# Kernel tuning notes

Hardware: AMD Instinct MI355X
Metric: run time of the kernel (lower is better)

## Reference

```python
import jax, jax.numpy as jnp
import numpy as np

N_NODES = 50000
N_EDGES = 800000
F_IN = 16
F_EDGE = 8
H = 8  # latent_dim = [8, 8]
NUM_GRAPHS = 512


def setup_inputs() -> dict:
    key = jax.random.key(0)
    ks = jax.random.split(key, 16)
    x = jax.random.normal(ks[0], (N_NODES, F_IN), dtype=jnp.float32)
    edge_index = jax.random.randint(ks[1], (2, N_EDGES), 0, N_NODES)
    edge_attr = jax.random.normal(ks[2], (N_EDGES, F_EDGE), dtype=jnp.float32)
    batch = jnp.sort(jax.random.randint(ks[3], (N_NODES,), 0, NUM_GRAPHS))
    s = 0.1
    # edge MLPs (single Linear each): edge_attr -> flattened [in, out] weight
    We1 = jax.random.normal(ks[4], (F_EDGE, F_IN * H), dtype=jnp.float32) * s
    be1 = jnp.zeros((F_IN * H,), dtype=jnp.float32)
    We2 = jax.random.normal(ks[5], (F_EDGE, H * H), dtype=jnp.float32) * s
    be2 = jnp.zeros((H * H,), dtype=jnp.float32)
    # NNConv root weights + biases
    root1 = jax.random.normal(ks[6], (F_IN, H), dtype=jnp.float32) * s
    b1 = jnp.zeros((H,), dtype=jnp.float32)
    root2 = jax.random.normal(ks[7], (H, H), dtype=jnp.float32) * s
    b2 = jnp.zeros((H,), dtype=jnp.float32)
    # final readout linear H -> 1
    Wlast = jax.random.normal(ks[8], (H, 1), dtype=jnp.float32) * s
    blast = jnp.zeros((1,), dtype=jnp.float32)
    return {"x": x, "edge_index": edge_index, "edge_attr": edge_attr, "batch": batch,
            "We1": We1, "be1": be1, "root1": root1, "b1": b1,
            "We2": We2, "be2": be2, "root2": root2, "b2": b2,
            "Wlast": Wlast, "blast": blast}


def _nnconv(x, src, dst, edge_attr, We, be, root, b, in_dim, out_dim):
    # per-edge weight matrix from edge MLP: [E, in_dim, out_dim]
    W = (edge_attr @ We + be).reshape(-1, in_dim, out_dim)
    # gather source features, per-edge matvec, scatter-add to targets
    msg = jnp.einsum('ei,eio->eo', x[src], W)            # [E, out_dim]
    agg = jax.ops.segment_sum(msg, dst, num_segments=x.shape[0])
    return agg + x @ root + b                            # root weight + bias


def reference(x, edge_index, edge_attr, batch, We1, be1, root1, b1,
              We2, be2, root2, b2, Wlast, blast):
    src, dst = edge_index[0], edge_index[1]
    h = jax.nn.relu(_nnconv(x, src, dst, edge_attr, We1, be1, root1, b1, F_IN, H))
    h = jax.nn.relu(_nnconv(h, src, dst, edge_attr, We2, be2, root2, b2, H, H))
    # per-graph sum pooling (vectorized equivalent of the python loop)
    pooled = jax.ops.segment_sum(h, batch, num_segments=NUM_GRAPHS)  # [G, H]
    return pooled @ Wlast + blast                                    # [G, 1]
```

## Files before the change

kernel.cpp:

```cpp
#include <hip/hip_runtime.h>
#include <hip/hip_fp16.h>

#define F_EDGE 8
#define H 8

__device__ __forceinline__ unsigned short f2bf(float f) {
    unsigned u = __float_as_uint(f);
    unsigned r = u + 0x7fffu + ((u >> 16) & 1u);
    return (unsigned short)(r >> 16);
}
__device__ __forceinline__ float bflo(unsigned u) { return __uint_as_float(u << 16); }
__device__ __forceinline__ float bfhi(unsigned u) { return __uint_as_float(u & 0xffff0000u); }

__global__ void init_out_kernel(float* __restrict__ out,
                                const float* __restrict__ blast, int n) {
    int g = blockIdx.x * blockDim.x + threadIdx.x;
    if (g < n) out[g] = blast[0];
}

__global__ __launch_bounds__(256) void pack_edges_kernel(
    const int* __restrict__ ei, const float* __restrict__ ea,
    uint2* __restrict__ rec, int E) {
    int e = blockIdx.x * blockDim.x + threadIdx.x;
    if (e >= E) return;
    uint2 hdr;
    hdr.x = (unsigned)ei[e];
    hdr.y = (unsigned)ei[E + e];
    const float4* av = (const float4*)(ea + (size_t)e * F_EDGE);
    float4 a0 = av[0], a1 = av[1];
    uint2 p0, p1;
    p0.x = (unsigned)f2bf(a0.x) | ((unsigned)f2bf(a0.y) << 16);
    p0.y = (unsigned)f2bf(a0.z) | ((unsigned)f2bf(a0.w) << 16);
    p1.x = (unsigned)f2bf(a1.x) | ((unsigned)f2bf(a1.y) << 16);
    p1.y = (unsigned)f2bf(a1.z) | ((unsigned)f2bf(a1.w) << 16);
    size_t b = (size_t)e * 3;
    rec[b] = hdr;
    rec[b + 1] = p0;
    rec[b + 2] = p1;
}

template <int IN, bool RELU, bool F16IN>
__global__ __launch_bounds__(256) void prep_kernel(
    const void* __restrict__ featv, const float* __restrict__ We,
    const float* __restrict__ be, const float* __restrict__ root,
    const float* __restrict__ b, unsigned short* __restrict__ Pt,
    float* __restrict__ q, __half* __restrict__ seedh, int n_nodes) {
    __shared__ float sW[IN * H * 12];
    int tid = threadIdx.x;
    for (int t = tid; t < IN * H * 12; t += 256) {
        int r = t / 12, m = t - r * 12;
        float v = 0.f;
        if (m < 8) v = We[m * (IN * H) + r];
        else if (m == 8) v = be[r];
        else if (m == 9) v = root[r];
        sW[t] = v;
    }
    __syncthreads();

    int n = blockIdx.x * 32 + (tid >> 3);
    if (n >= n_nodes) return;
    int j = tid & 7;

    float f[IN];
    if (F16IN) {
        const uint4* fv = (const uint4*)((const unsigned short*)featv + (size_t)n * IN);
        uint4 v = fv[0];
        unsigned w[4] = {v.x, v.y, v.z, v.w};
#pragma unroll
        for (int p = 0; p < 4 && 2 * p + 1 < IN; ++p) {
            __half2 h2v = *(__half2*)&w[p];
            float2 ff = __half22float2(h2v);
            f[2 * p] = ff.x;
            f[2 * p + 1] = ff.y;
        }
    } else {
        const float4* fv = (const float4*)((const float*)featv + (size_t)n * IN);
#pragma unroll
        for (int i4 = 0; i4 < IN / 4; ++i4) {
            float4 v = fv[i4];
            f[i4 * 4 + 0] = v.x; f[i4 * 4 + 1] = v.y;
            f[i4 * 4 + 2] = v.z; f[i4 * 4 + 3] = v.w;
        }
    }
    if (RELU) {
#pragma unroll
        for (int i = 0; i < IN; ++i) f[i] = f[i] > 0.f ? f[i] : 0.f;
    }

    float p[8] = {0.f, 0.f, 0.f, 0.f, 0.f, 0.f, 0.f, 0.f};
    float qq = 0.f, hr = 0.f;
#pragma unroll
    for (int i = 0; i < IN; ++i) {
        const float* row = &sW[(i * 8 + j) * 12];
        float4 w0 = *(const float4*)row;
        float4 w1 = *(const float4*)(row + 4);
        float2 br = *(const float2*)(row + 8);
        float fi = f[i];
        p[0] = fmaf(fi, w0.x, p[0]); p[1] = fmaf(fi, w0.y, p[1]);
        p[2] = fmaf(fi, w0.z, p[2]); p[3] = fmaf(fi, w0.w, p[3]);
        p[4] = fmaf(fi, w1.x, p[4]); p[5] = fmaf(fi, w1.y, p[5]);
        p[6] = fmaf(fi, w1.z, p[6]); p[7] = fmaf(fi, w1.w, p[7]);
        qq = fmaf(fi, br.x, qq);
        hr = fmaf(fi, br.y, hr);
    }
    uint4 pw;
    pw.x = (unsigned)f2bf(p[0]) | ((unsigned)f2bf(p[1]) << 16);
    pw.y = (unsigned)f2bf(p[2]) | ((unsigned)f2bf(p[3]) << 16);
    pw.z = (unsigned)f2bf(p[4]) | ((unsigned)f2bf(p[5]) << 16);
    pw.w = (unsigned)f2bf(p[6]) | ((unsigned)f2bf(p[7]) << 16);
    *(uint4*)(Pt + ((long long)n * H + j) * F_EDGE) = pw;
    q[(long long)n * H + j] = qq;
    seedh[(long long)n * H + j] = __float2half(hr + b[j]);
}

__global__ __launch_bounds__(256) void edge_fact_kernel(
    const uint2* __restrict__ rec,
    const unsigned short* __restrict__ Pt,
    const float* __restrict__ q,
    __half* __restrict__ agg,
    int E) {
    long long gid = (long long)blockIdx.x * blockDim.x + threadIdx.x;
    int e = (int)(gid >> 2);
    if (e >= E) return;
    int jj = (int)(gid & 3);

    size_t rb = (size_t)e * 3;
    uint2 hdr = rec[rb];
    uint2 A = rec[rb + 1];
    uint2 B = rec[rb + 2];
    int src = (int)hdr.x;
    int dst = (int)hdr.y;

    float a0 = bflo(A.x), a1 = bfhi(A.x), a2 = bflo(A.y), a3 = bfhi(A.y);
    float a4 = bflo(B.x), a5 = bfhi(B.x), a6 = bflo(B.y), a7 = bfhi(B.y);

    const uint4* pp = (const uint4*)(Pt + (size_t)src * 64 + jj * 16);
    uint4 lo = pp[0];
    uint4 hi = pp[1];

    float2 q2 = *(const float2*)(q + (size_t)src * H + jj * 2);

    float m0 = q2.x;
    m0 = fmaf(a0, bflo(lo.x), m0); m0 = fmaf(a1, bfhi(lo.x), m0);
    m0 = fmaf(a2, bflo(lo.y), m0); m0 = fmaf(a3, bfhi(lo.y), m0);
    m0 = fmaf(a4, bflo(lo.z), m0); m0 = fmaf(a5, bfhi(lo.z), m0);
    m0 = fmaf(a6, bflo(lo.w), m0); m0 = fmaf(a7, bfhi(lo.w), m0);

    float m1 = q2.y;
    m1 = fmaf(a0, bflo(hi.x), m1); m1 = fmaf(a1, bfhi(hi.x), m1);
    m1 = fmaf(a2, bflo(hi.y), m1); m1 = fmaf(a3, bfhi(hi.y), m1);
    m1 = fmaf(a4, bflo(hi.z), m1); m1 = fmaf(a5, bfhi(hi.z), m1);
    m1 = fmaf(a6, bflo(hi.w), m1); m1 = fmaf(a7, bfhi(hi.w), m1);

    __half2* ap = (__half2*)agg + ((size_t)dst * 4 + jj);
    unsafeAtomicAdd(ap, __floats2half2_rn(m0, m1));
}

__global__ __launch_bounds__(256) void pool_kernel(
    const unsigned short* __restrict__ h2, const int* __restrict__ batch,
    const float* __restrict__ Wlast, float* __restrict__ out,
    int n_nodes, int n_graphs) {
    __shared__ float bins[512];
    bool use_bins = (n_graphs <= 512);
    if (use_bins) {
        for (int t = threadIdx.x; t < n_graphs; t += 256) bins[t] = 0.f;
        __syncthreads();
    }
    float wl[8];
#pragma unroll
    for (int j = 0; j < 8; ++j) wl[j] = Wlast[j];

    int base = blockIdx.x * 1024;
#pragma unroll
    for (int r = 0; r < 4; ++r) {
        int n = base + r * 256 + threadIdx.x;
        if (n < n_nodes) {
            uint4 v = *(const uint4*)(h2 + (size_t)n * H);
            unsigned w[4] = {v.x, v.y, v.z, v.w};
            float c = 0.f;
#pragma unroll
            for (int p = 0; p < 4; ++p) {
                float2 ff = __half22float2(*(__half2*)&w[p]);
                c = fmaf(fmaxf(ff.x, 0.f), wl[2 * p], c);
                c = fmaf(fmaxf(ff.y, 0.f), wl[2 * p + 1], c);
            }
            if (use_bins) atomicAdd(&bins[batch[n]], c);
            else unsafeAtomicAdd(&out[batch[n]], c);
        }
    }
    if (use_bins) {
        __syncthreads();
        for (int t = threadIdx.x; t < n_graphs; t += 256) {
            float v = bins[t];
            if (v != 0.f) unsafeAtomicAdd(&out[t], v);
        }
    }
}

extern "C" void kernel_launch(void* const* d_in, const int* in_sizes, int n_in,
                              void* d_out, int out_size, void* d_ws, size_t ws_size,
                              hipStream_t stream) {
    const float* x     = (const float*)d_in[0];
    const int*   ei    = (const int*)d_in[1];
    const float* ea    = (const float*)d_in[2];
    const int*   batch = (const int*)d_in[3];
    const float* We1   = (const float*)d_in[4];
    const float* be1   = (const float*)d_in[5];
    const float* root1 = (const float*)d_in[6];
    const float* b1    = (const float*)d_in[7];
    const float* We2   = (const float*)d_in[8];
    const float* be2   = (const float*)d_in[9];
    const float* root2 = (const float*)d_in[10];
    const float* b2    = (const float*)d_in[11];
    const float* Wlast = (const float*)d_in[12];
    const float* blast = (const float*)d_in[13];
    float* out = (float*)d_out;

    int n_nodes = in_sizes[0] / 16;
    int E = in_sizes[1] / 2;

    char* w = (char*)d_ws;
    auto carve = [&](size_t bytes) {
        char* p = w;
        w += (bytes + 15) & ~(size_t)15;
        return p;
    };
    unsigned short* Pt1 = (unsigned short*)carve((size_t)n_nodes * 64 * 2);
    unsigned short* Pt2 = (unsigned short*)carve((size_t)n_nodes * 64 * 2);
    float* q1 = (float*)carve((size_t)n_nodes * 8 * 4);
    float* q2 = (float*)carve((size_t)n_nodes * 8 * 4);
    __half* h1 = (__half*)carve((size_t)n_nodes * 8 * 2);
    __half* h2 = (__half*)carve((size_t)n_nodes * 8 * 2);
    uint2* rec = (uint2*)carve((size_t)E * 24);

    init_out_kernel<<<(out_size + 255) / 256, 256, 0, stream>>>(out, blast, out_size);

    pack_edges_kernel<<<(E + 255) / 256, 256, 0, stream>>>(ei, ea, rec, E);

    int nblocks = (n_nodes + 31) / 32;
    prep_kernel<16, false, false><<<nblocks, 256, 0, stream>>>(
        x, We1, be1, root1, b1, Pt1, q1, h1, n_nodes);

    long long lanes = (long long)E * 4;
    int eblks = (int)((lanes + 255) / 256);
    edge_fact_kernel<<<eblks, 256, 0, stream>>>(rec, Pt1, q1, h1, E);

    prep_kernel<8, true, true><<<nblocks, 256, 0, stream>>>(
        h1, We2, be2, root2, b2, Pt2, q2, h2, n_nodes);

    edge_fact_kernel<<<eblks, 256, 0, stream>>>(rec, Pt2, q2, h2, E);

    pool_kernel<<<(n_nodes + 1023) / 1024, 256, 0, stream>>>(
        (const unsigned short*)h2, batch, Wlast, out, n_nodes, out_size);
}
```

Before: 206.1 us.

## Bucket edges by source-node range to localize gathers per XCD

```diff
diff --git a/kernel.cpp b/kernel.cpp
--- a/kernel.cpp
+++ b/kernel.cpp
@@ -3,6 +3,7 @@
 
 #define F_EDGE 8
 #define H 8
+#define NBUCKET 8
 
 __device__ __forceinline__ unsigned short f2bf(float f) {
     unsigned u = __float_as_uint(f);
@@ -18,25 +19,54 @@
     if (g < n) out[g] = blast[0];
 }
 
-__global__ __launch_bounds__(256) void pack_edges_kernel(
+__global__ void zero_small_kernel(int* __restrict__ p, int n) {
+    int i = threadIdx.x;
+    if (i < n) p[i] = 0;
+}
+
+__global__ __launch_bounds__(256) void bucket_pack_kernel(
     const int* __restrict__ ei, const float* __restrict__ ea,
-    uint2* __restrict__ rec, int E) {
-    int e = blockIdx.x * blockDim.x + threadIdx.x;
-    if (e >= E) return;
-    uint2 hdr;
-    hdr.x = (unsigned)ei[e];
-    hdr.y = (unsigned)ei[E + e];
-    const float4* av = (const float4*)(ea + (size_t)e * F_EDGE);
-    float4 a0 = av[0], a1 = av[1];
+    int* __restrict__ gcount,
+    uint2* __restrict__ recs,
+    int E, int n_nodes, int cap) {
+    __shared__ int cnt[NBUCKET];
+    __shared__ int base[NBUCKET];
+    int tid = threadIdx.x;
+    if (tid < NBUCKET) cnt[tid] = 0;
+    __syncthreads();
+
+    int e = blockIdx.x * 256 + tid;
+    bool valid = e < E;
+    int b = 0, r = 0, src = 0, dst = 0;
     uint2 p0, p1;
-    p0.x = (unsigned)f2bf(a0.x) | ((unsigned)f2bf(a0.y) << 16);
-    p0.y = (unsigned)f2bf(a0.z) | ((unsigned)f2bf(a0.w) << 16);
-    p1.x = (unsigned)f2bf(a1.x) | ((unsigned)f2bf(a1.y) << 16);
-    p1.y = (unsigned)f2bf(a1.z) | ((unsigned)f2bf(a1.w) << 16);
-    size_t b = (size_t)e * 3;
-    rec[b] = hdr;
-    rec[b + 1] = p0;
-    rec[b + 2] = p1;
+    if (valid) {
+        src = ei[e];
+        dst = ei[E + e];
+        b = (int)(((unsigned long long)(unsigned)src * NBUCKET) / (unsigned)n_nodes);
+        r = atomicAdd(&cnt[b], 1);
+        const float4* av = (const float4*)(ea + (size_t)e * F_EDGE);
+        float4 a0 = av[0], a1 = av[1];
+        p0.x = (unsigned)f2bf(a0.x) | ((unsigned)f2bf(a0.y) << 16);
+        p0.y = (unsigned)f2bf(a0.z) | ((unsigned)f2bf(a0.w) << 16);
+        p1.x = (unsigned)f2bf(a1.x) | ((unsigned)f2bf(a1.y) << 16);
+        p1.y = (unsigned)f2bf(a1.z) | ((unsigned)f2bf(a1.w) << 16);
+    }
+    __syncthreads();
+    if (tid < NBUCKET)
+        base[tid] = (cnt[tid] > 0) ? atomicAdd(&gcount[tid], cnt[tid]) : 0;
+    __syncthreads();
+    if (valid) {
+        int pos = base[b] + r;
+        if (pos < cap) {
+            size_t rb = ((size_t)b * cap + pos) * 3;
+            uint2 hdr;
+            hdr.x = (unsigned)src;
+            hdr.y = (unsigned)dst;
+            recs[rb] = hdr;
+            recs[rb + 1] = p0;
+            recs[rb + 2] = p1;
+        }
+    }
 }
 
 template <int IN, bool RELU, bool F16IN>
@@ -114,20 +144,23 @@
 }
 
 __global__ __launch_bounds__(256) void edge_fact_kernel(
-    const uint2* __restrict__ rec,
+    const uint2* __restrict__ recs,
+    const int* __restrict__ gcount,
     const unsigned short* __restrict__ Pt,
     const float* __restrict__ q,
     __half* __restrict__ agg,
-    int E) {
-    long long gid = (long long)blockIdx.x * blockDim.x + threadIdx.x;
-    int e = (int)(gid >> 2);
-    if (e >= E) return;
-    int jj = (int)(gid & 3);
-
-    size_t rb = (size_t)e * 3;
-    uint2 hdr = rec[rb];
-    uint2 A = rec[rb + 1];
-    uint2 B = rec[rb + 2];
+    int cap) {
+    int bucket = blockIdx.x & 7;
+    int lblk = blockIdx.x >> 3;
+    int cnt = gcount[bucket];
+    int el = lblk * 64 + (threadIdx.x >> 2);
+    if (el >= cnt) return;
+    int jj = threadIdx.x & 3;
+
+    size_t rb = ((size_t)bucket * cap + el) * 3;
+    uint2 hdr = recs[rb];
+    uint2 A = recs[rb + 1];
+    uint2 B = recs[rb + 2];
     int src = (int)hdr.x;
     int dst = (int)hdr.y;
 
@@ -218,6 +251,7 @@
 
     int n_nodes = in_sizes[0] / 16;
     int E = in_sizes[1] / 2;
+    int cap = E / NBUCKET + 4096;
 
     char* w = (char*)d_ws;
     auto carve = [&](size_t bytes) {
@@ -231,24 +265,27 @@
     float* q2 = (float*)carve((size_t)n_nodes * 8 * 4);
     __half* h1 = (__half*)carve((size_t)n_nodes * 8 * 2);
     __half* h2 = (__half*)carve((size_t)n_nodes * 8 * 2);
-    uint2* rec = (uint2*)carve((size_t)E * 24);
+    int* gcount = (int*)carve(NBUCKET * 4);
+    uint2* recs = (uint2*)carve((size_t)NBUCKET * cap * 24);
 
     init_out_kernel<<<(out_size + 255) / 256, 256, 0, stream>>>(out, blast, out_size);
-
-    pack_edges_kernel<<<(E + 255) / 256, 256, 0, stream>>>(ei, ea, rec, E);
+    zero_small_kernel<<<1, 64, 0, stream>>>(gcount, NBUCKET);
+
+    bucket_pack_kernel<<<(E + 255) / 256, 256, 0, stream>>>(
+        ei, ea, gcount, recs, E, n_nodes, cap);
 
     int nblocks = (n_nodes + 31) / 32;
     prep_kernel<16, false, false><<<nblocks, 256, 0, stream>>>(
         x, We1, be1, root1, b1, Pt1, q1, h1, n_nodes);
 
-    long long lanes = (long long)E * 4;
-    int eblks = (int)((lanes + 255) / 256);
-    edge_fact_kernel<<<eblks, 256, 0, stream>>>(rec, Pt1, q1, h1, E);
+    int bpb = (cap + 63) / 64;
+    int eblks = bpb * NBUCKET;
+    edge_fact_kernel<<<eblks, 256, 0, stream>>>(recs, gcount, Pt1, q1, h1, cap);
 
     prep_kernel<8, true, true><<<nblocks, 256, 0, stream>>>(
         h1, We2, be2, root2, b2, Pt2, q2, h2, n_nodes);
 
-    edge_fact_kernel<<<eblks, 256, 0, stream>>>(rec, Pt2, q2, h2, E);
+    edge_fact_kernel<<<eblks, 256, 0, stream>>>(recs, gcount, Pt2, q2, h2, cap);
 
     pool_kernel<<<(n_nodes + 1023) / 1024, 256, 0, stream>>>(
         (const unsigned short*)h2, batch, Wlast, out, n_nodes, out_size);
```

Result: slower. 238.4 us (+15.7%).
